# Performance work log

Measured on AMD Instinct MI355X. Metric: run time of the kernel, lower is better.

## Reference

```python
import jax, jax.numpy as jnp
import numpy as np

NH, NP = 8, 4  # n_heads, n_points
SHAPES = [(100, 167), (50, 84), (25, 42), (13, 21)]  # (H, W) per level


def setup_inputs() -> dict:
    key = jax.random.key(0)
    ks = jax.random.split(key, 8)
    bs, dm = 2, 256
    nl = len(SHAPES)
    nv = sum(h * w for h, w in SHAPES)  # 22223
    nq = nv
    s = 1.0 / np.sqrt(dm)
    return {
        'query': jax.random.normal(ks[0], (bs, nq, dm), jnp.float32),
        'value': jax.random.normal(ks[1], (bs, nv, dm), jnp.float32),
        'reference_points': jax.random.uniform(ks[2], (bs, nq, nl, 2), jnp.float32),
        'W_so': jax.random.normal(ks[3], (dm, NH * nl * NP * 2), jnp.float32) * 0.01,
        'b_so': jax.random.normal(ks[4], (NH * nl * NP * 2,), jnp.float32) * 0.5,
        'W_aw': jax.random.normal(ks[5], (dm, NH * nl * NP), jnp.float32) * s,
        'b_aw': jnp.zeros((NH * nl * NP,), jnp.float32),
        'W_vp': jax.random.normal(ks[6], (dm, dm), jnp.float32) * s,
        'b_vp': jnp.zeros((dm,), jnp.float32),
        'W_op': jax.random.normal(ks[7], (dm, dm), jnp.float32) * s,
        'b_op': jnp.zeros((dm,), jnp.float32),
        'spatial_shapes': jnp.array(SHAPES, jnp.int32),
    }


def _bilinear_gather(vf, H, W, loc):
    # vf: [BH, H*W, dh] flattened level feature map; loc: [BH, QP, 2] in [0,1]
    # Matches torch grid_sample(mode='bilinear', padding_mode='zeros', align_corners=False)
    x = loc[..., 0] * W - 0.5
    y = loc[..., 1] * H - 0.5
    x0f = jnp.floor(x); y0f = jnp.floor(y)
    lx = x - x0f; ly = y - y0f
    x0 = x0f.astype(jnp.int32); y0 = y0f.astype(jnp.int32)
    out = jnp.zeros(vf.shape[:1] + loc.shape[1:2] + vf.shape[-1:], vf.dtype)
    for dx, dy, w in ((0, 0, (1 - lx) * (1 - ly)), (1, 0, lx * (1 - ly)),
                      (0, 1, (1 - lx) * ly), (1, 1, lx * ly)):
        xi = x0 + dx; yi = y0 + dy
        valid = (xi >= 0) & (xi < W) & (yi >= 0) & (yi < H)
        idx = jnp.clip(yi, 0, H - 1) * W + jnp.clip(xi, 0, W - 1)  # [BH, QP]
        g = jnp.take_along_axis(vf, idx[:, :, None], axis=1)  # [BH, QP, dh]
        out = out + g * (w * valid)[:, :, None]
    return out


def _msda(value_heads, shapes_np, loc, aw):
    # value_heads: [bs,nv,nh,dh], loc: [bs,nq,nh,nl,np,2], aw: [bs,nq,nh,nl,np]
    bs, nv, nh, dh = value_heads.shape
    nq, nl, npnt = loc.shape[1], loc.shape[3], loc.shape[4]
    out = jnp.zeros((bs * nh, nq, dh), value_heads.dtype)
    start = 0
    for lvl in range(nl):
        H, W = int(shapes_np[lvl, 0]), int(shapes_np[lvl, 1])
        vf = value_heads[:, start:start + H * W].transpose(0, 2, 1, 3).reshape(bs * nh, H * W, dh)
        loc_l = loc[:, :, :, lvl].transpose(0, 2, 1, 3, 4).reshape(bs * nh, nq * npnt, 2)
        samp = _bilinear_gather(vf, H, W, loc_l).reshape(bs * nh, nq, npnt, dh)
        aw_l = aw[:, :, :, lvl].transpose(0, 2, 1, 3).reshape(bs * nh, nq, npnt)
        out = out + jnp.einsum('bqpd,bqp->bqd', samp, aw_l)
        start += H * W
    return out.reshape(bs, nh, nq, dh).transpose(0, 2, 1, 3).reshape(bs, nq, nh * dh)


def reference(query, value, reference_points, W_so, b_so, W_aw, b_aw, W_vp, b_vp, W_op, b_op, spatial_shapes):
    bs, nq, dm = query.shape
    nl = reference_points.shape[2]
    dh = dm // NH
    v = (value @ W_vp + b_vp).reshape(bs, value.shape[1], NH, dh)
    off = (query @ W_so + b_so).reshape(bs, nq, NH, nl, NP, 2)
    aw = jax.nn.softmax((query @ W_aw + b_aw).reshape(bs, nq, NH, nl * NP), axis=-1)
    aw = aw.reshape(bs, nq, NH, nl, NP)
    ss = np.asarray(spatial_shapes)  # static level metadata
    normalizer = jnp.asarray(np.stack([ss[:, 1], ss[:, 0]], -1), query.dtype)  # (w, h) per level
    loc = reference_points[:, :, None, :, None, :] + off / normalizer[None, None, None, :, None, :]
    out = _msda(v, ss, loc, aw)
    return out @ W_op + b_op + query  # identity residual (identity defaults to query)
```

## Files before the change

kernel.cpp:

```cpp
#include <hip/hip_runtime.h>
#include <hip/hip_bf16.h>
#include <math.h>

typedef __hip_bfloat16 bf16;
using f32x4  = __attribute__((ext_vector_type(4))) float;
using f32x2  = __attribute__((ext_vector_type(2))) float;
using bf16x8 = __attribute__((ext_vector_type(8))) short;
using f16x2  = __attribute__((ext_vector_type(2))) _Float16;

constexpr int BS = 2, NQ = 22223, MROWS = 44446;
constexpr int LH[4] = {100, 50, 25, 13};
constexpr int LW[4] = {167, 84, 42, 21};
constexpr int LSTART[4] = {0, 16700, 20900, 21950};
constexpr int PLW[4] = {170, 87, 45, 24};
constexpr int PLSTART[4] = {0, 17510, 22121, 23381};
constexpr int PTOT = 23765;

constexpr int BM = 128, BK = 32;
constexpr int LDT = 40;
constexpr int GX = (MROWS + BM - 1) / BM;

__global__ __launch_bounds__(256) void prep_weights(
    const float* __restrict__ W_vp, const float* __restrict__ W_so,
    const float* __restrict__ W_aw, const float* __restrict__ W_op,
    const float* __restrict__ b_so, const float* __restrict__ b_aw,
    bf16* __restrict__ Wt_vp, bf16* __restrict__ Wt_cat,
    bf16* __restrict__ Wt_op, float* __restrict__ bcat)
{
    int i = blockIdx.x * 256 + threadIdx.x;
    if (i < 256 * 256) {
        int n = i >> 8, k = i & 255;
        Wt_vp[i] = __float2bfloat16(W_vp[k * 256 + n]);
        Wt_op[i] = __float2bfloat16(W_op[k * 256 + n]);
    }
    if (i < 384 * 256) {
        int n = i >> 8, k = i & 255;
        float v = (n < 256) ? W_so[k * 256 + n] : W_aw[k * 128 + (n - 256)];
        Wt_cat[i] = __float2bfloat16(v);
    }
    if (i < 384) bcat[i] = (i < 256) ? b_so[i] : b_aw[i - 256];
}

__device__ inline int pad_base_idx(int pix) {
    if (pix < LSTART[1])      { int y = pix / 167;                  int x = pix - y * 167;                return PLSTART[0] + (y + 1) * 170 + (x + 1); }
    else if (pix < LSTART[2]) { int rel = pix - LSTART[1]; int y = rel / 84; int x = rel - y * 84;        return PLSTART[1] + (y + 1) * 87  + (x + 1); }
    else if (pix < LSTART[3]) { int rel = pix - LSTART[2]; int y = rel / 42; int x = rel - y * 42;        return PLSTART[2] + (y + 1) * 45  + (x + 1); }
    else                      { int rel = pix - LSTART[3]; int y = rel / 21; int x = rel - y * 21;        return PLSTART[3] + (y + 1) * 24  + (x + 1); }
}

template<bool A_BF16>
__device__ __forceinline__ void mfma_core(
    const void* __restrict__ Av, int lda, const bf16* __restrict__ Wt,
    int row0, int bn0, int M, bf16* As, bf16* Bs, f32x4 (&acc)[4][4])
{
    const int tid = threadIdx.x;
    const int lane = tid & 63;
    const int wv = tid >> 6;
    const int wm = (wv >> 1) * 64, wn = (wv & 1) * 64;
    const int l15 = lane & 15, l4 = lane >> 4;

#pragma unroll
    for (int m = 0; m < 4; ++m)
#pragma unroll
        for (int n = 0; n < 4; ++n) { acc[m][n][0]=0.f; acc[m][n][1]=0.f; acc[m][n][2]=0.f; acc[m][n][3]=0.f; }

    for (int k0 = 0; k0 < 256; k0 += BK) {
        __syncthreads();
#pragma unroll
        for (int t = 0; t < 2; ++t) {
            int idx = tid + t * 256;
            int r = idx >> 2, s = idx & 3;
            {
                int grow = row0 + r; if (grow >= M) grow = M - 1;
                bf16 tmp[8];
                if constexpr (A_BF16) {
                    const bf16* ap = (const bf16*)Av + (size_t)grow * lda + (k0 + s * 8);
                    *(uint4*)tmp = *(const uint4*)ap;
                } else {
                    const float* ap = (const float*)Av + (size_t)grow * lda + (k0 + s * 8);
                    f32x4 v0 = *(const f32x4*)ap;
                    f32x4 v1 = *(const f32x4*)(ap + 4);
#pragma unroll
                    for (int j = 0; j < 4; ++j) tmp[j] = __float2bfloat16(v0[j]);
#pragma unroll
                    for (int j = 0; j < 4; ++j) tmp[4 + j] = __float2bfloat16(v1[j]);
                }
                *(uint4*)&As[r * LDT + s * 8] = *(const uint4*)tmp;
            }
            *(uint4*)&Bs[r * LDT + s * 8] =
                *(const uint4*)(Wt + (size_t)(bn0 + r) * 256 + (k0 + s * 8));
        }
        __syncthreads();

        bf16x8 af[4], bfr[4];
#pragma unroll
        for (int m = 0; m < 4; ++m)
            af[m] = *(const bf16x8*)&As[(wm + m * 16 + l15) * LDT + l4 * 8];
#pragma unroll
        for (int n = 0; n < 4; ++n)
            bfr[n] = *(const bf16x8*)&Bs[(wn + n * 16 + l15) * LDT + l4 * 8];
#pragma unroll
        for (int m = 0; m < 4; ++m)
#pragma unroll
            for (int n = 0; n < 4; ++n)
                acc[m][n] = __builtin_amdgcn_mfma_f32_16x16x32_bf16(af[m], bfr[n], acc[m][n], 0, 0, 0);
    }
}

__global__ __launch_bounds__(256) void gemm_producer(
    const float* __restrict__ query, const float* __restrict__ value,
    const bf16* __restrict__ Wt_cat, const bf16* __restrict__ Wt_vp,
    const float* __restrict__ bcat, const float* __restrict__ bvp,
    bf16* __restrict__ offawl, _Float16* __restrict__ vproj)
{
    __shared__ bf16 As[BM * LDT];
    __shared__ bf16 Bs[BM * LDT];

    constexpr int NWG = GX * 5;
    constexpr int QXW = NWG / 8, RXW = NWG % 8;
    int orig = blockIdx.x;
    int xcd = orig & 7, seq = orig >> 3;
    int swz = (xcd < RXW ? xcd * (QXW + 1) : RXW * (QXW + 1) + (xcd - RXW) * QXW) + seq;
    int slice = swz % 5;
    int row0 = (swz / 5) * BM;

    const bool isOff = slice < 3;
    const void* A = isOff ? (const void*)query : (const void*)value;
    const bf16* Wt = isOff ? Wt_cat : Wt_vp;
    const float* bias = isOff ? bcat : bvp;
    int bn0 = isOff ? slice * 128 : (slice - 3) * 128;

    f32x4 acc[4][4];
    mfma_core<false>(A, 256, Wt, row0, bn0, MROWS, As, Bs, acc);

    const int lane = threadIdx.x & 63;
    const int wv = threadIdx.x >> 6;
    const int wm = (wv >> 1) * 64, wn = (wv & 1) * 64;
    const int l15 = lane & 15, l4 = lane >> 4;

    if (isOff) {
#pragma unroll
        for (int m = 0; m < 4; ++m)
#pragma unroll
            for (int j = 0; j < 4; ++j) {
                int r = row0 + wm + m * 16 + l4 * 4 + j;
                if (r < MROWS) {
                    bf16* orow = offawl + (size_t)r * 384;
#pragma unroll
                    for (int n = 0; n < 4; ++n) {
                        int fcol = bn0 + wn + n * 16 + l15;
                        orow[fcol] = __float2bfloat16(acc[m][n][j] + bias[fcol]);
                    }
                }
            }
    } else {
#pragma unroll
        for (int m = 0; m < 4; ++m)
#pragma unroll
            for (int j = 0; j < 4; ++j) {
                int r = row0 + wm + m * 16 + l4 * 4 + j;
                if (r < MROWS) {
                    int bb = (r >= NQ) ? 1 : 0;
                    int pb = pad_base_idx(r - bb * NQ);
#pragma unroll
                    for (int n = 0; n < 4; ++n) {
                        int fcol = bn0 + wn + n * 16 + l15;
                        int hh = fcol >> 5, cc = fcol & 31;
                        vproj[((size_t)(hh * 2 + bb) * PTOT + pb) * 32 + cc] =
                            (_Float16)(acc[m][n][j] + bias[fcol]);
                    }
                }
            }
    }
}

__global__ __launch_bounds__(256) void gemm_out(
    const bf16* __restrict__ msda, const bf16* __restrict__ Wt_op,
    const float* __restrict__ b_op, const float* __restrict__ query,
    float* __restrict__ out)
{
    __shared__ bf16 As[BM * LDT];
    __shared__ bf16 Bs[BM * LDT];

    constexpr int NWG = GX * 2;
    int orig = blockIdx.x;
    int swz = (orig & 7) * (NWG / 8) + (orig >> 3);
    int bn0 = (swz & 1) * 128;
    int row0 = (swz >> 1) * BM;

    f32x4 acc[4][4];
    mfma_core<true>(msda, 384, Wt_op, row0, bn0, MROWS, As, Bs, acc);

    const int lane = threadIdx.x & 63;
    const int wv = threadIdx.x >> 6;
    const int wm = (wv >> 1) * 64, wn = (wv & 1) * 64;
    const int l15 = lane & 15, l4 = lane >> 4;

#pragma unroll
    for (int m = 0; m < 4; ++m)
#pragma unroll
        for (int j = 0; j < 4; ++j) {
            int r = row0 + wm + m * 16 + l4 * 4 + j;
            if (r < MROWS) {
#pragma unroll
                for (int n = 0; n < 4; ++n) {
                    int fcol = bn0 + wn + n * 16 + l15;
                    out[(size_t)r * 256 + fcol] =
                        acc[m][n][j] + b_op[fcol] + query[(size_t)r * 256 + fcol];
                }
            }
        }
}

__device__ inline f32x2 bfpair(unsigned u) {
    f32x2 r;
    r.x = __uint_as_float(u << 16);
    r.y = __uint_as_float(u & 0xffff0000u);
    return r;
}

__global__ __launch_bounds__(256)
__attribute__((amdgpu_waves_per_eu(2, 4)))
void msda_sample16(
    const _Float16* __restrict__ vproj,
    const bf16* __restrict__ offawl,
    const float* __restrict__ refp,
    bf16* __restrict__ msda_out)
{
    __shared__ uint2 sOA[4][96];
    __shared__ float sRef[4][8];

    constexpr int NBLK = (MROWS + 3) / 4;
    const int orig = blockIdx.x;
    const int blk = (orig & 7) * (NBLK / 8) + (orig >> 3);
    const int q0 = blk * 4;

    const int tid = threadIdx.x;

#pragma unroll
    for (int k = 0; k < 2; ++k) {
        int idx = tid + k * 256;
        if (idx < 384) {
            int row = idx / 96, e = idx - (idx / 96) * 96;
            int grow = min(q0 + row, MROWS - 1);
            sOA[row][e] = *((const uint2*)(offawl + (size_t)grow * 384) + e);
        }
    }
    if (tid < 32) {
        int row = tid >> 3, er = tid & 7;
        int grow = min(q0 + row, MROWS - 1);
        sRef[row][er] = refp[(size_t)grow * 8 + er];
    }
    __syncthreads();

    const int w = tid >> 6;
    const int lane = tid & 63;
    const int h = lane >> 3;
    const int s = lane & 7;
    const int sx = s >> 2;
    const int c16 = s & 3;
    int q = q0 + w;
    const bool alive = q < MROWS;
    if (!alive) q = MROWS - 1;
    const int b = (q >= NQ) ? 1 : 0;

    const char* rowp = (const char*)&sOA[w][0];

    float aw0, aw1;
    {
        unsigned lgu = *(const unsigned*)(rowp + 512 + h * 32 + s * 4);
        f32x2 lg = bfpair(lgu);
        float m = fmaxf(lg.x, lg.y);
        m = fmaxf(m, __shfl_xor(m, 1));
        m = fmaxf(m, __shfl_xor(m, 2));
        m = fmaxf(m, __shfl_xor(m, 4));
        float e0 = __expf(lg.x - m), e1 = __expf(lg.y - m);
        float ssum = e0 + e1;
        ssum += __shfl_xor(ssum, 1);
        ssum += __shfl_xor(ssum, 2);
        ssum += __shfl_xor(ssum, 4);
        float inv = 1.f / ssum;
        aw0 = e0 * inv;
        aw1 = e1 * inv;
    }

    int rpix0, rpix1;
    int rw00, rw10, rw01, rw11;
    {
        const int lo = s >> 1;
        const int Wl  = (lo == 0) ? 167 : (lo == 1) ? 84 : (lo == 2) ? 42 : 21;
        const int Hl  = (lo == 0) ? 100 : (lo == 1) ? 50 : (lo == 2) ? 25 : 13;
        const int Wpl = (lo == 0) ? 170 : (lo == 1) ? 87 : (lo == 2) ? 45 : 24;
        const float xb = sRef[w][lo * 2 + 0] * (float)Wl + 0.5f;
        const float yb = sRef[w][lo * 2 + 1] * (float)Hl + 0.5f;
        uint2 ou = *(const uint2*)(rowp + h * 64 + s * 8);
        unsigned ouv[2] = {ou.x, ou.y};
        float awv[2] = {aw0, aw1};
        int pixv[2]; int w0v[2], w1v[2];
#pragma unroll
        for (int k = 0; k < 2; ++k) {
            f32x2 o2 = bfpair(ouv[k]);
            float x = fminf(fmaxf(xb + o2.x, 0.f), (float)(Wl + 1));
            float y = fminf(fmaxf(yb + o2.y, 0.f), (float)(Hl + 1));
            float x0f = floorf(x), y0f = floorf(y);
            float lx = x - x0f, ly = y - y0f;
            float a = awv[k];
            float wy0 = (1.f - ly) * a, wy1 = ly * a;
            float wx0 = 1.f - lx;
            pixv[k] = ((int)y0f * Wpl + (int)x0f) * 32;
            w0v[k] = (int)__builtin_bit_cast(unsigned,
                        f16x2{(_Float16)(wx0 * wy0), (_Float16)(wx0 * wy1)});
            w1v[k] = (int)__builtin_bit_cast(unsigned,
                        f16x2{(_Float16)(lx * wy0), (_Float16)(lx * wy1)});
        }
        rpix0 = pixv[0]; rw00 = w0v[0]; rw10 = w1v[0];
        rpix1 = pixv[1]; rw01 = w0v[1]; rw11 = w1v[1];
    }

    const int srcbase = lane & 56;
    f16x2 acc0 = {0, 0}, acc1 = {0, 0}, acc2 = {0, 0}, acc3 = {0, 0};

#pragma unroll
    for (int l = 0; l < 4; ++l) {
        const int Wp = PLW[l];
        const _Float16* vl = vproj + ((size_t)(h * 2 + b) * PTOT + PLSTART[l]) * 32
                             + sx * 32 + c16 * 8;

        const _Float16* pr[4][2];
        f16x2 hw0[4], hw1[4];
#pragma unroll
        for (int p = 0; p < 4; ++p) {
            const int t = l * 4 + p;
            const int src = srcbase | (t >> 1);
            int pix, wa, wb;
            if (t & 1) {
                pix = __shfl(rpix1, src);
                wa  = __shfl(rw01, src);
                wb  = __shfl(rw11, src);
            } else {
                pix = __shfl(rpix0, src);
                wa  = __shfl(rw00, src);
                wb  = __shfl(rw10, src);
            }
            f16x2 wv = __builtin_bit_cast(f16x2, (unsigned)(sx ? wb : wa));
            hw0[p] = f16x2{wv[0], wv[0]};
            hw1[p] = f16x2{wv[1], wv[1]};
            pr[p][0] = vl + pix;
            pr[p][1] = pr[p][0] + Wp * 32;
        }

        uint4 c[4][2];
#pragma unroll
        for (int p = 0; p < 4; ++p) {
            c[p][0] = *(const uint4*)pr[p][0];
            c[p][1] = *(const uint4*)pr[p][1];
        }

#pragma unroll
        for (int p = 0; p < 4; ++p) {
            acc0 += __builtin_bit_cast(f16x2, c[p][0].x) * hw0[p];
            acc1 += __builtin_bit_cast(f16x2, c[p][0].y) * hw0[p];
            acc2 += __builtin_bit_cast(f16x2, c[p][0].z) * hw0[p];
            acc3 += __builtin_bit_cast(f16x2, c[p][0].w) * hw0[p];
            acc0 += __builtin_bit_cast(f16x2, c[p][1].x) * hw1[p];
            acc1 += __builtin_bit_cast(f16x2, c[p][1].y) * hw1[p];
            acc2 += __builtin_bit_cast(f16x2, c[p][1].z) * hw1[p];
            acc3 += __builtin_bit_cast(f16x2, c[p][1].w) * hw1[p];
        }
    }

    {
        unsigned u0 = __builtin_bit_cast(unsigned, acc0);
        unsigned u1 = __builtin_bit_cast(unsigned, acc1);
        unsigned u2 = __builtin_bit_cast(unsigned, acc2);
        unsigned u3 = __builtin_bit_cast(unsigned, acc3);
        acc0 += __builtin_bit_cast(f16x2, __shfl_xor((int)u0, 4));
        acc1 += __builtin_bit_cast(f16x2, __shfl_xor((int)u1, 4));
        acc2 += __builtin_bit_cast(f16x2, __shfl_xor((int)u2, 4));
        acc3 += __builtin_bit_cast(f16x2, __shfl_xor((int)u3, 4));
    }

    if (alive && sx == 0) {
        bf16 ob[8];
        ob[0] = __float2bfloat16((float)acc0[0]);
        ob[1] = __float2bfloat16((float)acc0[1]);
        ob[2] = __float2bfloat16((float)acc1[0]);
        ob[3] = __float2bfloat16((float)acc1[1]);
        ob[4] = __float2bfloat16((float)acc2[0]);
        ob[5] = __float2bfloat16((float)acc2[1]);
        ob[6] = __float2bfloat16((float)acc3[0]);
        ob[7] = __float2bfloat16((float)acc3[1]);
        *(uint4*)(msda_out + (size_t)q * 384 + h * 32 + c16 * 8) = *(const uint4*)ob;
    }
}

extern "C" void kernel_launch(void* const* d_in, const int* in_sizes, int n_in,
                              void* d_out, int out_size, void* d_ws, size_t ws_size,
                              hipStream_t stream) {
    const float* query = (const float*)d_in[0];
    const float* value = (const float*)d_in[1];
    const float* refp  = (const float*)d_in[2];
    const float* W_so  = (const float*)d_in[3];
    const float* b_so  = (const float*)d_in[4];
    const float* W_aw  = (const float*)d_in[5];
    const float* b_aw  = (const float*)d_in[6];
    const float* W_vp  = (const float*)d_in[7];
    const float* b_vp  = (const float*)d_in[8];
    const float* W_op  = (const float*)d_in[9];
    const float* b_op  = (const float*)d_in[10];
    float* out = (float*)d_out;

    bf16*     d_offawl = (bf16*)d_ws;
    _Float16* d_vproj  = (_Float16*)(d_offawl + (size_t)MROWS * 384);
    bf16*     d_wtcat  = (bf16*)(d_vproj + (size_t)16 * PTOT * 32);
    bf16*     d_wtvp   = d_wtcat + 384 * 256;
    bf16*     d_wtop   = d_wtvp + 256 * 256;
    float*    d_bcat   = (float*)(d_wtop + 256 * 256);

    prep_weights<<<384, 256, 0, stream>>>(W_vp, W_so, W_aw, W_op, b_so, b_aw,
                                          d_wtvp, d_wtcat, d_wtop, d_bcat);
    hipMemsetAsync(d_vproj, 0, (size_t)16 * PTOT * 32 * sizeof(_Float16), stream);

    gemm_producer<<<GX * 5, 256, 0, stream>>>(
        query, value, d_wtcat, d_wtvp, d_bcat, b_vp, d_offawl, d_vproj);

    msda_sample16<<<(MROWS + 3) / 4, 256, 0, stream>>>(
        d_vproj, d_offawl, refp, d_offawl);

    gemm_out<<<GX * 2, 256, 0, stream>>>(d_offawl, d_wtop, b_op, query, out);
}
```

Measured before the change: 147.9 us.

## Remap sampling blocks to one head per block over 32 queries

The sampling kernel now gives each block a single head and 32 queries, where before each block handled all 8 heads of 4 queries. Lanes within a wave now index queries instead of heads. Grid order interleaves heads (blockIdx & 7), so concurrent blocks touch all heads over nearby queries, while each block's gathers stay inside one head's value plane. This aims to improve cache locality of the bilinear gathers. The cost is strided, smaller loads of offsets and logits per row and the loss of the earlier block-swizzle ordering.

Result: faster. 138.4 us (-6.4%).

```diff
diff --git a/kernel.cpp b/kernel.cpp
--- a/kernel.cpp
+++ b/kernel.cpp
@@ -221,54 +221,48 @@
 
 __global__ __launch_bounds__(256)
 __attribute__((amdgpu_waves_per_eu(2, 4)))
-void msda_sample16(
+void msda_sample18(
     const _Float16* __restrict__ vproj,
     const bf16* __restrict__ offawl,
     const float* __restrict__ refp,
     bf16* __restrict__ msda_out)
 {
-    __shared__ uint2 sOA[4][96];
-    __shared__ float sRef[4][8];
-
-    constexpr int NBLK = (MROWS + 3) / 4;
-    const int orig = blockIdx.x;
-    const int blk = (orig & 7) * (NBLK / 8) + (orig >> 3);
-    const int q0 = blk * 4;
+    __shared__ uint2 sOff[32][8];
+    __shared__ uint2 sAwl[32][4];
+    __shared__ float sRef[32][8];
 
     const int tid = threadIdx.x;
-
-#pragma unroll
-    for (int k = 0; k < 2; ++k) {
-        int idx = tid + k * 256;
-        if (idx < 384) {
-            int row = idx / 96, e = idx - (idx / 96) * 96;
-            int grow = min(q0 + row, MROWS - 1);
-            sOA[row][e] = *((const uint2*)(offawl + (size_t)grow * 384) + e);
-        }
-    }
-    if (tid < 32) {
-        int row = tid >> 3, er = tid & 7;
-        int grow = min(q0 + row, MROWS - 1);
-        sRef[row][er] = refp[(size_t)grow * 8 + er];
+    const int head = blockIdx.x & 7;
+    const int qbase = (blockIdx.x >> 3) * 32;
+
+    {
+        int row = tid >> 3, e = tid & 7;
+        int grow = min(qbase + row, MROWS - 1);
+        sOff[row][e] = *((const uint2*)(offawl + (size_t)grow * 384 + head * 32) + e);
+        sRef[row][e] = refp[(size_t)grow * 8 + e];
+        if (tid < 128) {
+            int rowa = tid >> 2, ea = tid & 3;
+            int growa = min(qbase + rowa, MROWS - 1);
+            sAwl[rowa][ea] = *((const uint2*)(offawl + (size_t)growa * 384 + 256 + head * 16) + ea);
+        }
     }
     __syncthreads();
 
     const int w = tid >> 6;
     const int lane = tid & 63;
-    const int h = lane >> 3;
+    const int ql = lane >> 3;
     const int s = lane & 7;
     const int sx = s >> 2;
     const int c16 = s & 3;
-    int q = q0 + w;
+    const int lq = w * 8 + ql;
+    int q = qbase + lq;
     const bool alive = q < MROWS;
     if (!alive) q = MROWS - 1;
     const int b = (q >= NQ) ? 1 : 0;
 
-    const char* rowp = (const char*)&sOA[w][0];
-
     float aw0, aw1;
     {
-        unsigned lgu = *(const unsigned*)(rowp + 512 + h * 32 + s * 4);
+        unsigned lgu = ((const unsigned*)&sAwl[lq][0])[s];
         f32x2 lg = bfpair(lgu);
         float m = fmaxf(lg.x, lg.y);
         m = fmaxf(m, __shfl_xor(m, 1));
@@ -291,9 +285,9 @@
         const int Wl  = (lo == 0) ? 167 : (lo == 1) ? 84 : (lo == 2) ? 42 : 21;
         const int Hl  = (lo == 0) ? 100 : (lo == 1) ? 50 : (lo == 2) ? 25 : 13;
         const int Wpl = (lo == 0) ? 170 : (lo == 1) ? 87 : (lo == 2) ? 45 : 24;
-        const float xb = sRef[w][lo * 2 + 0] * (float)Wl + 0.5f;
-        const float yb = sRef[w][lo * 2 + 1] * (float)Hl + 0.5f;
-        uint2 ou = *(const uint2*)(rowp + h * 64 + s * 8);
+        const float xb = sRef[lq][lo * 2 + 0] * (float)Wl + 0.5f;
+        const float yb = sRef[lq][lo * 2 + 1] * (float)Hl + 0.5f;
+        uint2 ou = sOff[lq][s];
         unsigned ouv[2] = {ou.x, ou.y};
         float awv[2] = {aw0, aw1};
         int pixv[2]; int w0v[2], w1v[2];
@@ -323,7 +317,7 @@
 #pragma unroll
     for (int l = 0; l < 4; ++l) {
         const int Wp = PLW[l];
-        const _Float16* vl = vproj + ((size_t)(h * 2 + b) * PTOT + PLSTART[l]) * 32
+        const _Float16* vl = vproj + ((size_t)(head * 2 + b) * PTOT + PLSTART[l]) * 32
                              + sx * 32 + c16 * 8;
 
         const _Float16* pr[4][2];
@@ -390,7 +384,7 @@
         ob[5] = __float2bfloat16((float)acc2[1]);
         ob[6] = __float2bfloat16((float)acc3[0]);
         ob[7] = __float2bfloat16((float)acc3[1]);
-        *(uint4*)(msda_out + (size_t)q * 384 + h * 32 + c16 * 8) = *(const uint4*)ob;
+        *(uint4*)(msda_out + (size_t)q * 384 + head * 32 + c16 * 8) = *(const uint4*)ob;
     }
 }
 
@@ -424,7 +418,7 @@
     gemm_producer<<<GX * 5, 256, 0, stream>>>(
         query, value, d_wtcat, d_wtvp, d_bcat, b_vp, d_offawl, d_vproj);
 
-    msda_sample16<<<(MROWS + 3) / 4, 256, 0, stream>>>(
+    msda_sample18<<<8 * ((MROWS + 31) / 32), 256, 0, stream>>>(
         d_vproj, d_offawl, refp, d_offawl);
 
     gemm_out<<<GX * 2, 256, 0, stream>>>(d_offawl, d_wtop, b_op, query, out);
```
